# Performance work log

Hardware: AMD Instinct MI355X
Metric: run time of the kernel (lower is better)

The kernel has to match this reference:

```python
import jax, jax.numpy as jnp
import numpy as np

USAGE_DECAY = 0.99
EPS = 1e-12


def _addressing(key, beta, gate, shift, gamma, prev_w, memory, half_shift):
    # key [B,M], beta/gate/gamma [B,1], shift [B,K], prev_w [B,N], memory [B,N,M]
    kn = key / (jnp.linalg.norm(key, axis=-1, keepdims=True) + EPS)
    mn = memory / (jnp.linalg.norm(memory, axis=-1, keepdims=True) + EPS)
    cos = jnp.einsum('bnm,bm->bn', mn, kn)                      # [B,N]
    beta_p = jax.nn.softplus(beta[:, 0])
    wc = jax.nn.softmax(beta_p[:, None] * cos, axis=-1)
    g = jax.nn.sigmoid(gate[:, 0])[:, None]
    wg = g * wc + (1.0 - g) * prev_w
    s = jax.nn.softmax(shift, axis=-1)                          # [B,K]
    K = shift.shape[-1]
    shifted = sum(s[:, k:k + 1] * jnp.roll(wg, k - half_shift, axis=-1) for k in range(K))
    gamma_p = 1.0 + jax.nn.softplus(gamma[:, 0])
    wt = (shifted + EPS) ** gamma_p[:, None]
    return wt / (wt.sum(axis=-1, keepdims=True) + EPS)


def _allocate(usage):
    # faithful to source: cumprod over zero-prepended shifted usage
    sorted_u = jnp.sort(usage, axis=-1)
    free = jnp.argsort(usage, axis=-1)
    shifted = jnp.concatenate([jnp.zeros_like(sorted_u[:, :1]), sorted_u[:, :-1]], axis=-1)
    aw = (1.0 - sorted_u) * jnp.cumprod(shifted, axis=-1)
    B = usage.shape[0]
    return jnp.zeros_like(usage).at[jnp.arange(B)[:, None], free].set(aw)


def _forward(ctrl, read_W, read_b, write_W, write_b,
             memory0, link0, precedence0, usage0, read_w0, write_w0):
    T, B, D = ctrl.shape
    N, M = memory0.shape[1], memory0.shape[2]
    RH, WH = read_w0.shape[1], write_w0.shape[1]
    rpl = read_W.shape[0] // RH   # M + K + 6
    wpl = write_W.shape[0] // WH  # 3M + K + 4
    K = rpl - M - 6
    half = K // 2
    eye = jnp.eye(N, dtype=memory0.dtype)

    def step(carry, ctrl_t):
        memory, link, prec, usage, read_w, write_w = carry
        rp = (ctrl_t @ read_W.T + read_b).reshape(B, RH, rpl)
        wp = (ctrl_t @ write_W.T + write_b).reshape(B, WH, wpl)

        # ---- write heads: content addr + allocation, erase/add, temporal links ----
        new_write = []
        for h in range(WH):
            p = wp[:, h]
            key = p[:, :M]
            beta = p[:, M:M + 1]
            gate = p[:, M + 1:M + 2]
            shift = p[:, M + 2:M + 2 + K]
            gamma = p[:, M + 2 + K:M + 3 + K]
            erase = jax.nn.sigmoid(p[:, M + 3 + K:2 * M + 3 + K])
            add = p[:, 2 * M + 3 + K:3 * M + 3 + K]
            a_gate = jax.nn.sigmoid(p[:, 3 * M + 3 + K:])          # [B,1]
            w_addr = _addressing(key, beta, gate, shift, gamma, write_w[:, h], memory, half)
            alloc = _allocate(usage)
            w = a_gate * alloc + (1.0 - a_gate) * w_addr           # [B,N]
            memory = memory * (1.0 - w[:, :, None] * erase[:, None, :]) + w[:, :, None] * add[:, None, :]
            link = (1.0 - w[:, :, None]) * link + prec[:, :, None] * w[:, None, :]
            link = link * (1.0 - eye)[None]
            # faithful to source: sum over dim 0 (batch)
            prec = (1.0 - w.sum(axis=0, keepdims=True)) * prec + w
            usage = jnp.clip(USAGE_DECAY * usage + w, 0.0, 1.0)
            new_write.append(w)
        write_w = jnp.stack(new_write, axis=1)

        # ---- read heads: content + forward/backward temporal link modes ----
        new_read, reads = [], []
        for h in range(RH):
            p = rp[:, h]
            key = p[:, :M]
            beta = p[:, M:M + 1]
            gate = p[:, M + 1:M + 2]
            shift = p[:, M + 2:M + 2 + K]
            gamma = p[:, M + 2 + K:M + 3 + K]
            pi = jax.nn.softmax(p[:, M + 3 + K:M + 6 + K], axis=-1)  # [B,3] back/content/fwd
            wc = _addressing(key, beta, gate, shift, gamma, read_w[:, h], memory, half)
            fwd = jnp.einsum('bn,bnk->bk', read_w[:, h], link)
            bwd = jnp.einsum('bn,bkn->bk', read_w[:, h], link)
            w = pi[:, 0:1] * bwd + pi[:, 1:2] * wc + pi[:, 2:3] * fwd
            new_read.append(w)
            reads.append(jnp.einsum('bn,bnm->bm', w, memory))
        read_w = jnp.stack(new_read, axis=1)
        reads = jnp.stack(reads, axis=1)                            # [B,RH,M]
        return (memory, link, prec, usage, read_w, write_w), reads

    carry0 = (memory0, link0, precedence0, usage0, read_w0, write_w0)
    _, reads = jax.lax.scan(step, carry0, ctrl)
    return reads  # [T,B,RH,M]


def setup_inputs() -> dict:
    key = jax.random.key(0)
    ks = jax.random.split(key, 8)
    T, B, D = 32, 4, 256
    N, M = 1024, 256
    RH, WH, K = 1, 1, 3
    rpl = M + K + 6
    wpl = 3 * M + K + 4
    ctrl = jax.random.normal(ks[0], (T, B, D), dtype=jnp.float32)
    read_W = jax.random.normal(ks[1], (RH * rpl, D), dtype=jnp.float32) * 0.05
    read_b = jnp.zeros((RH * rpl,), dtype=jnp.float32)
    write_W = jax.random.normal(ks[2], (WH * wpl, D), dtype=jnp.float32) * 0.05
    write_b = jnp.zeros((WH * wpl,), dtype=jnp.float32)
    memory0 = jax.random.normal(ks[3], (B, N, M), dtype=jnp.float32) * 0.1
    link0 = jnp.zeros((B, N, N), dtype=jnp.float32)
    precedence0 = jnp.zeros((B, N), dtype=jnp.float32)
    usage0 = jax.random.uniform(ks[4], (B, N), dtype=jnp.float32)
    read_w0 = jnp.zeros((B, RH, N), dtype=jnp.float32).at[:, :, 0].set(1.0)
    write_w0 = jnp.zeros((B, WH, N), dtype=jnp.float32).at[:, :, 0].set(1.0)
    return {"ctrl": ctrl, "read_W": read_W, "read_b": read_b,
            "write_W": write_W, "write_b": write_b, "memory0": memory0,
            "link0": link0, "precedence0": precedence0, "usage0": usage0,
            "read_w0": read_w0, "write_w0": write_w0}


def reference(ctrl, read_W, read_b, write_W, write_b, memory0, link0,
              precedence0, usage0, read_w0, write_w0):
    return _forward(ctrl, read_W, read_b, write_W, write_b,
                    memory0, link0, precedence0, usage0, read_w0, write_w0)
```

## Files before the change

kernel.cpp:

```cpp
#include <hip/hip_runtime.h>

#define GRID 128
#define TPB 256
#define SLICE 32
#define BB 4
#define DD 256
#define NN 1024
#define MM 256
#define KSH 3
#define RPL 265
#define WPL 775
#define TS 32
#define EPSF 1e-12f

struct KArgs {
    const float *ctrl, *rW, *rb, *wW, *wb;
    const float *memory0, *prec0, *read_w0, *write_w0;
    float *out;
    float *rp, *wp;
    float *cosr, *cosw, *wbuf, *rdw;
    float *csp, *dsp;
    float *rdp;
    unsigned *flagsA, *flagsB;
};

__device__ __forceinline__ float cload(const float* p){
    return __hip_atomic_load(p, __ATOMIC_RELAXED, __HIP_MEMORY_SCOPE_SYSTEM);
}
__device__ __forceinline__ void cstore(float* p, float v){
    __hip_atomic_store(p, v, __ATOMIC_RELAXED, __HIP_MEMORY_SCOPE_SYSTEM);
}

__device__ __forceinline__ float softplusf(float x){
    return fmaxf(x, 0.0f) + log1pf(expf(-fabsf(x)));
}
__device__ __forceinline__ float sigmoidf(float x){
    return 1.0f / (1.0f + expf(-x));
}

template <bool FENCE>
__device__ __forceinline__ void garrive(unsigned* flags, unsigned gen, int g, int tid){
    __syncthreads();
    if (tid == 0){
        if (FENCE) __builtin_amdgcn_fence(__ATOMIC_RELEASE, "agent");
        __hip_atomic_store(&flags[g*16], gen, __ATOMIC_RELAXED, __HIP_MEMORY_SCOPE_SYSTEM);
    }
}
template <bool FENCE>
__device__ __forceinline__ void gwait(unsigned* flags, unsigned gen, int tid){
    if (tid < 64){
        while (1){
            unsigned f0 = __hip_atomic_load(&flags[tid*16], __ATOMIC_RELAXED, __HIP_MEMORY_SCOPE_SYSTEM);
            unsigned f1 = __hip_atomic_load(&flags[(tid+64)*16], __ATOMIC_RELAXED, __HIP_MEMORY_SCOPE_SYSTEM);
            if (__all(f0 >= gen && f1 >= gen)) break;
            __builtin_amdgcn_s_sleep(1);
        }
    }
    __syncthreads();
    if (FENCE) __builtin_amdgcn_fence(__ATOMIC_ACQUIRE, "agent");
    asm volatile("" ::: "memory");
}
__device__ __forceinline__ void gwaitA(unsigned* flags, unsigned gen, int b, int tid){
    if (tid < 64){
        int idx = b*32 + (tid & 31);
        while (1){
            unsigned f0 = __hip_atomic_load(&flags[idx*16], __ATOMIC_RELAXED, __HIP_MEMORY_SCOPE_SYSTEM);
            if (__all(f0 >= gen)) break;
            __builtin_amdgcn_s_sleep(1);
        }
    }
    __syncthreads();
    asm volatile("" ::: "memory");
}

__device__ __forceinline__ float blk_sum(float v, float* s4, int tid){
    #pragma unroll
    for (int off = 32; off; off >>= 1) v += __shfl_down(v, off);
    if ((tid & 63) == 0) s4[tid >> 6] = v;
    __syncthreads();
    float r = s4[0] + s4[1] + s4[2] + s4[3];
    __syncthreads();
    return r;
}

__device__ __forceinline__ float half_sum(float v, float* slots, int htid){
    #pragma unroll
    for (int off = 32; off; off >>= 1) v += __shfl_down(v, off);
    if ((htid & 63) == 0) slots[htid >> 6] = v;
    __syncthreads();
    float r = slots[0] + slots[1];
    __syncthreads();
    return r;
}

__device__ __forceinline__ void addr_core2(const float cosx[4], const float prev[4],
                                           const float* __restrict__ p,
                                           float* s4, float* wg, int tid,
                                           float out_wc[4]){
    float beta_p  = softplusf(p[MM]);
    float g       = sigmoidf(p[MM+1]);
    float s0r = p[MM+2], s1r = p[MM+3], s2r = p[MM+4];
    float smx = fmaxf(s0r, fmaxf(s1r, s2r));
    float e0 = expf(s0r-smx), e1 = expf(s1r-smx), e2 = expf(s2r-smx);
    float sden = e0+e1+e2;
    float s0 = e0/sden, s1 = e1/sden, s2 = e2/sden;
    float gamma_p = 1.0f + softplusf(p[MM+2+KSH]);
    float ev[4]; float ls = 0.0f;
    #pragma unroll
    for (int q = 0; q < 4; q++){ ev[q] = expf(beta_p*cosx[q] - beta_p); ls += ev[q]; }
    float bs = blk_sum(ls, s4, tid);
    float invb = 1.0f / bs;
    #pragma unroll
    for (int q = 0; q < 4; q++){
        int i = tid + q*256;
        wg[i] = g*(ev[q]*invb) + (1.0f-g)*prev[q];
    }
    __syncthreads();
    float wt[4]; float lps = 0.0f;
    #pragma unroll
    for (int q = 0; q < 4; q++){
        int i = tid + q*256;
        float sh = s0*wg[(i+1)&(NN-1)] + s1*wg[i] + s2*wg[(i-1)&(NN-1)];
        wt[q] = exp2f(gamma_p * log2f(sh + EPSF));
        lps += wt[q];
    }
    float ts = blk_sum(lps, s4, tid);
    float inv = 1.0f / (ts + EPSF);
    #pragma unroll
    for (int q = 0; q < 4; q++) out_wc[q] = wt[q] * inv;
    __syncthreads();
}

__device__ __forceinline__ void addr_half(const float cosx[8], const float prev[8],
                                          const float* __restrict__ p,
                                          float* swg, float* slots,
                                          int htid, float out_wc[8]){
    float beta_p  = softplusf(p[MM]);
    float g       = sigmoidf(p[MM+1]);
    float s0r = p[MM+2], s1r = p[MM+3], s2r = p[MM+4];
    float smx = fmaxf(s0r, fmaxf(s1r, s2r));
    float e0 = expf(s0r-smx), e1 = expf(s1r-smx), e2 = expf(s2r-smx);
    float sden = e0+e1+e2;
    float s0 = e0/sden, s1 = e1/sden, s2 = e2/sden;
    float gamma_p = 1.0f + softplusf(p[MM+2+KSH]);

    float ev[8]; float ls = 0.0f;
    #pragma unroll
    for (int q = 0; q < 8; q++){ ev[q] = expf(beta_p*cosx[q] - beta_p); ls += ev[q]; }
    float bs = half_sum(ls, slots, htid);
    float invb = 1.0f / bs;
    #pragma unroll
    for (int q = 0; q < 8; q++){
        int i = htid + q*128;
        swg[i] = g*(ev[q]*invb) + (1.0f-g)*prev[q];
    }
    __syncthreads();
    float wt[8]; float lps = 0.0f;
    #pragma unroll
    for (int q = 0; q < 8; q++){
        int i = htid + q*128;
        float sh = s0*swg[(i+1)&(NN-1)] + s1*swg[i] + s2*swg[(i-1)&(NN-1)];
        wt[q] = exp2f(gamma_p * log2f(sh + EPSF));
        lps += wt[q];
    }
    float ts2 = half_sum(lps, slots, htid);
    float inv = 1.0f / (ts2 + EPSF);
    #pragma unroll
    for (int q = 0; q < 8; q++) out_wc[q] = wt[q] * inv;
    __syncthreads();
}

__device__ __forceinline__ void tail_cos(const KArgs& a, int tnext, int b, int g, int ns0,
        float (*lmem)[MM], float (*skey)[MM],
        const float* lwn, const float* rdvec, int tid){
    if (rdvec){
        float accv = 0.f;
        #pragma unroll 8
        for (int j = 0; j < SLICE; j++) accv += rdvec[j]*lmem[j][tid];
        cstore(&a.rdp[(size_t)((tnext-1)&1)*GRID*MM + g*MM + tid], accv);
    }
    const float* kr = a.rp + (size_t)tnext*BB*RPL + (size_t)b*RPL;
    const bool hw = (tnext+1 <= TS-1);
    const float* kwp = a.wp + (size_t)(hw ? tnext+1 : tnext)*BB*WPL + (size_t)b*WPL;
    skey[0][tid] = kr[tid];
    skey[1][tid] = kwp[tid];
    __syncthreads();
    {
        const float* pw = a.wp + (size_t)tnext*BB*WPL + (size_t)b*WPL;
        float e = pw[MM+3+KSH + tid];
        float d = pw[2*MM+3+KSH + tid];
        #pragma unroll 8
        for (int j = 0; j < SLICE; j++){
            float w = lwn[j];
            lmem[j][tid] = lmem[j][tid]*(1.0f - w*e) + w*d;
        }
    }
    __syncthreads();
    {
        int j = tid >> 3, c = tid & 7;
        float dr=0.f, dw=0.f, nm=0.f, nr=0.f, nk=0.f;
        #pragma unroll
        for (int m = 0; m < 8; m++){
            int col = c*4 + m*32;
            float4 mv = *(const float4*)&lmem[j][col];
            float4 rv = *(const float4*)&skey[0][col];
            float4 wv = *(const float4*)&skey[1][col];
            dr += mv.x*rv.x + mv.y*rv.y + mv.z*rv.z + mv.w*rv.w;
            dw += mv.x*wv.x + mv.y*wv.y + mv.z*wv.z + mv.w*wv.w;
            nm += mv.x*mv.x + mv.y*mv.y + mv.z*mv.z + mv.w*mv.w;
            nr += rv.x*rv.x + rv.y*rv.y + rv.z*rv.z + rv.w*rv.w;
            nk += wv.x*wv.x + wv.y*wv.y + wv.z*wv.z + wv.w*wv.w;
        }
        #pragma unroll
        for (int off = 4; off; off >>= 1){
            dr += __shfl_down(dr, off); dw += __shfl_down(dw, off);
            nm += __shfl_down(nm, off); nr += __shfl_down(nr, off);
            nk += __shfl_down(nk, off);
        }
        if (c == 0){
            float sn = sqrtf(nm) + EPSF;
            int n = ns0 + j;
            cstore(&a.cosr[(size_t)(tnext&1)*BB*NN + b*NN + n], dr/(sn*(sqrtf(nr)+EPSF)));
            if (hw) cstore(&a.cosw[(size_t)((tnext+1)&1)*BB*NN + b*NN + n], dw/(sn*(sqrtf(nk)+EPSF)));
        }
    }
}

__device__ __forceinline__ void tail_links(const KArgs& a, int tnext, int g,
        float (*lA)[SLICE], float (*lW)[SLICE],
        const float* lwn, const float* rvec, const float* lprec, int tid){
    for (int p2 = tid; p2 < tnext*SLICE; p2 += TPB){
        int s = p2 >> 5, jj = p2 & 31;
        lA[s][jj] *= (1.0f - lwn[jj]);
    }
    __syncthreads();
    if (tid < SLICE){ lA[tnext][tid] = lprec[tid]; lW[tnext][tid] = lwn[tid]; }
    __syncthreads();
    int s = tid >> 3, c = tid & 7;
    if (s <= tnext){
        float pc = 0.f, pd = 0.f;
        #pragma unroll
        for (int q = 0; q < 4; q++){
            int jj = c*4 + q;
            float r = rvec[jj];
            pc += r*lA[s][jj];
            pd += r*lW[s][jj];
        }
        #pragma unroll
        for (int off = 4; off; off >>= 1){ pc += __shfl_down(pc, off); pd += __shfl_down(pd, off); }
        if (c == 0){
            cstore(&a.csp[(size_t)(tnext&1)*GRID*TS + g*TS + s], pc);
            cstore(&a.dsp[(size_t)(tnext&1)*GRID*TS + g*TS + s], pd);
        }
    }
}

__global__ void __launch_bounds__(TPB) kfull(KArgs a){
    const int g   = blockIdx.x;
    const int tid = threadIdx.x;
    const int wvi = tid >> 6, lane = tid & 63;
    const int b   = g >> 5;
    const int sl  = g & 31;
    const int ns0 = sl * SLICE;
    const int sq    = sl >> 3;
    const int sbase = (sl & 7) * 32;
    const int hbase = ns0 & 127;
    const int qsl   = ns0 >> 7;

    __shared__ __align__(16) float lmem[SLICE][MM];
    __shared__ __align__(16) float skey[2][MM];
    __shared__ __align__(16) float lA[TS][SLICE];
    __shared__ __align__(16) float lW[TS][SLICE];
    __shared__ float wgA[NN], wgB[NN];
    __shared__ float s8[8];
    __shared__ float scs[TS], sds[TS];
    __shared__ float lprec[SLICE], lr_old[SLICE], lw_old[SLICE];
    __shared__ float lrn[SLICE], lwn[SLICE], lbw[SLICE], lfw[SLICE];

    {
        const int tt = g >> 2;
        for (int o = tid; o < BB*DD; o += TPB) wgA[o] = a.ctrl[(size_t)tt*BB*DD + o];
        __syncthreads();
        for (int half = 0; half < 2; half++){
            int jc = (g & 3) + half*4;
            int j = jc*130 + tid;
            if (tid < 130 && j < RPL + WPL){
                const float* wrow; float bias; int isw, jj;
                if (j < RPL){ jj = j;       wrow = a.rW + (size_t)jj*DD; bias = a.rb[jj]; isw = 0; }
                else        { jj = j - RPL; wrow = a.wW + (size_t)jj*DD; bias = a.wb[jj]; isw = 1; }
                const float4* w4 = (const float4*)wrow;
                float a0 = bias, a1 = bias, a2 = bias, a3 = bias;
                for (int d = 0; d < DD/4; d++){
                    float4 wv = w4[d];
                    float4 c0 = *(const float4*)&wgA[0*DD + d*4];
                    float4 c1 = *(const float4*)&wgA[1*DD + d*4];
                    float4 c2 = *(const float4*)&wgA[2*DD + d*4];
                    float4 c3 = *(const float4*)&wgA[3*DD + d*4];
                    a0 += wv.x*c0.x + wv.y*c0.y + wv.z*c0.z + wv.w*c0.w;
                    a1 += wv.x*c1.x + wv.y*c1.y + wv.z*c1.z + wv.w*c1.w;
                    a2 += wv.x*c2.x + wv.y*c2.y + wv.z*c2.z + wv.w*c2.w;
                    a3 += wv.x*c3.x + wv.y*c3.y + wv.z*c3.z + wv.w*c3.w;
                }
                if (isw && jj >= MM+3+KSH && jj < 2*MM+3+KSH){
                    a0 = sigmoidf(a0); a1 = sigmoidf(a1); a2 = sigmoidf(a2); a3 = sigmoidf(a3);
                }
                if (!isw){
                    float* dst = a.rp + (size_t)tt*BB*RPL;
                    dst[0*RPL+jj]=a0; dst[1*RPL+jj]=a1; dst[2*RPL+jj]=a2; dst[3*RPL+jj]=a3;
                } else {
                    float* dst = a.wp + (size_t)tt*BB*WPL;
                    dst[0*WPL+jj]=a0; dst[1*WPL+jj]=a1; dst[2*WPL+jj]=a2; dst[3*WPL+jj]=a3;
                }
            }
        }
    }
    garrive<true>(a.flagsA, 1, g, tid);
    gwait<true>(a.flagsA, 1, tid);

    {
        const float* kw = a.wp + (size_t)b*WPL;
        const int m0 = lane*4;
        float k0=kw[m0], k1=kw[m0+1], k2=kw[m0+2], k3=kw[m0+3];
        float nk = k0*k0 + k1*k1 + k2*k2 + k3*k3;
        #pragma unroll
        for (int off = 32; off; off >>= 1) nk += __shfl_down(nk, off);
        nk = __shfl(nk, 0);
        float snk = sqrtf(nk) + EPSF;
        for (int rr = 0; rr < 8; rr++){
            int j = wvi*8 + rr, n = ns0 + j;
            float4 m4 = ((const float4*)a.memory0)[((size_t)(b*NN+n))*64 + lane];
            *(float4*)&lmem[j][m0] = m4;
            float dw = m4.x*k0 + m4.y*k1 + m4.z*k2 + m4.w*k3;
            float nm = m4.x*m4.x + m4.y*m4.y + m4.z*m4.z + m4.w*m4.w;
            #pragma unroll
            for (int off = 32; off; off >>= 1){ dw += __shfl_down(dw, off); nm += __shfl_down(nm, off); }
            if (lane == 0) cstore(&a.cosw[0*BB*NN + b*NN + n], dw / ((sqrtf(nm)+EPSF)*snk));
        }
        if (tid < SLICE){
            lprec[tid]  = a.prec0[b*NN + ns0 + tid];
            lr_old[tid] = a.read_w0[b*NN + ns0 + tid];
        }
    }
    garrive<false>(a.flagsA, 2, g, tid);
    gwait<false>(a.flagsA, 2, tid);

    {
        const float* p = a.wp + (size_t)b*WPL;
        float cosx[4], prev[4], wcf[4];
        #pragma unroll
        for (int q = 0; q < 4; q++){
            int i = tid + q*256;
            cosx[q] = cload(&a.cosw[0*BB*NN + b*NN + i]);
            prev[q] = a.write_w0[b*NN + i];
        }
        addr_core2(cosx, prev, p, s8, wgA, tid, wcf);
        float ag = sigmoidf(p[3*MM+3+KSH]);
        if (tid >= sbase && tid < sbase+32){
            int j = tid - sbase;
            float v = (1.0f - ag)*wcf[sq];
            lwn[j] = v;
            cstore(&a.wbuf[0*BB*NN + b*NN + ns0 + j], v);
        }
        __syncthreads();
        tail_cos(a, 0, b, g, ns0, lmem, skey, lwn, nullptr, tid);
        garrive<false>(a.flagsA, 3, g, tid);
        tail_links(a, 0, g, lA, lW, lwn, lr_old, lprec, tid);
        garrive<false>(a.flagsB, 1, g, tid);
        __syncthreads();
        if (tid < SLICE) lw_old[tid] = lwn[tid];
    }

    for (int t = 0; t < TS; t++){
        const int cur = t & 1, nxt = cur ^ 1;
        const int half = wvi >> 1, htid = tid & 127;
        gwaitA(a.flagsA, 3 + t, b, tid);

        float cosx[8], prev[8];
        const float* addr_p;
        if (half == 0){
            addr_p = a.rp + (size_t)t*BB*RPL + (size_t)b*RPL;
            #pragma unroll
            for (int q = 0; q < 8; q++){
                int i = htid + q*128;
                cosx[q] = cload(&a.cosr[(size_t)cur*BB*NN + b*NN + i]);
                prev[q] = (t == 0) ? a.read_w0[b*NN + i]
                                   : cload(&a.rdw[(size_t)nxt*BB*NN + b*NN + i]);
            }
        } else {
            int tw = (t < TS-1) ? t+1 : t;
            addr_p = a.wp + (size_t)tw*BB*WPL + (size_t)b*WPL;
            #pragma unroll
            for (int q = 0; q < 8; q++){
                int i = htid + q*128;
                cosx[q] = cload(&a.cosw[(size_t)nxt*BB*NN + b*NN + i]);
                prev[q] = cload(&a.wbuf[(size_t)cur*BB*NN + b*NN + i]);
            }
        }

        gwait<false>(a.flagsB, 1 + t, tid);

        float cv[4] = {0,0,0,0}, dv[4] = {0,0,0,0};
        {
            int s = tid >> 3, c = tid & 7;
            if (s <= t){
                #pragma unroll
                for (int q = 0; q < 4; q++){
                    int slc = c + q*8;
                    cv[q] = cload(&a.csp[(size_t)cur*GRID*TS + (b*32+slc)*TS + s]);
                    dv[q] = cload(&a.dsp[(size_t)cur*GRID*TS + (b*32+slc)*TS + s]);
                }
            }
        }
        float rdpv = 0.f;
        if (t > 0)
            rdpv = cload(&a.rdp[(size_t)nxt*GRID*MM + (size_t)(b*32+(tid&31))*MM + sl*8 + (tid>>5)]);
        if (tid < SLICE){
            float wsum = 0.f;
            #pragma unroll
            for (int bq = 0; bq < BB; bq++)
                wsum += cload(&a.wbuf[(size_t)cur*BB*NN + bq*NN + ns0 + tid]);
            lprec[tid] = (1.0f - wsum)*lprec[tid] + lw_old[tid];
        }

        float wcf[8];
        addr_half(cosx, prev, addr_p,
                  (half == 0) ? wgA : wgB,
                  (half == 0) ? &s8[0] : &s8[2],
                  htid, wcf);

        {
            int s = tid >> 3, c = tid & 7;
            float pc = cv[0]+cv[1]+cv[2]+cv[3];
            float pd = dv[0]+dv[1]+dv[2]+dv[3];
            #pragma unroll
            for (int off = 4; off; off >>= 1){ pc += __shfl_down(pc, off); pd += __shfl_down(pd, off); }
            if (c == 0 && s <= t){ scs[s] = pc; sds[s] = pd; }
            if (t > 0){
                #pragma unroll
                for (int off = 16; off; off >>= 1) rdpv += __shfl_down(rdpv, off);
                if ((tid & 31) == 0) a.out[(size_t)(t-1)*BB*MM + b*MM + sl*8 + (tid>>5)] = rdpv;
            }
        }
        __syncthreads();
        if (tid < SLICE){
            float bwv = 0.f, fwv = 0.f, qq = 0.f;
            for (int s2 = 0; s2 <= t; s2++){
                float av = lA[s2][tid], wv = lW[s2][tid];
                qq  += av*wv;
                bwv += sds[s2]*av;
                fwv += scs[s2]*wv;
            }
            float corr = lr_old[tid]*qq;
            lbw[tid] = bwv - corr;
            lfw[tid] = fwv - corr;
        }
        __syncthreads();
        if (half == 0){
            float x0 = addr_p[MM+3+KSH], x1 = addr_p[MM+4+KSH], x2 = addr_p[MM+5+KSH];
            float mx = fmaxf(x0, fmaxf(x1, x2));
            float q0 = expf(x0-mx), q1 = expf(x1-mx), q2 = expf(x2-mx);
            float qs = q0+q1+q2;
            float pi0 = q0/qs, pi1 = q1/qs, pi2 = q2/qs;
            if (htid >= hbase && htid < hbase + 32){
                int j = htid - hbase;
                float v = pi0*lbw[j] + pi1*wcf[qsl] + pi2*lfw[j];
                lrn[j] = v;
                cstore(&a.rdw[(size_t)cur*BB*NN + b*NN + ns0 + j], v);
            }
        } else if (t < TS-1){
            float ag = sigmoidf(addr_p[3*MM+3+KSH]);
            if (htid >= hbase && htid < hbase + 32){
                int j = htid - hbase;
                float v = (1.0f - ag)*wcf[qsl];
                lwn[j] = v;
                cstore(&a.wbuf[(size_t)nxt*BB*NN + b*NN + ns0 + j], v);
            }
        }
        __syncthreads();

        if (t < TS-1){
            tail_cos(a, t+1, b, g, ns0, lmem, skey, lwn, lrn, tid);
            garrive<false>(a.flagsA, 4 + t, g, tid);
            tail_links(a, t+1, g, lA, lW, lwn, lrn, lprec, tid);
            garrive<false>(a.flagsB, 2 + t, g, tid);
            __syncthreads();
            if (tid < SLICE){ lr_old[tid] = lrn[tid]; lw_old[tid] = lwn[tid]; }
        } else {
            float accv = 0.f;
            #pragma unroll 8
            for (int j = 0; j < SLICE; j++) accv += lrn[j]*lmem[j][tid];
            cstore(&a.rdp[(size_t)1*GRID*MM + g*MM + tid], accv);
            garrive<false>(a.flagsB, 2 + t, g, tid);
        }
    }

    gwait<false>(a.flagsB, TS + 1, tid);
    {
        float v = cload(&a.rdp[(size_t)1*GRID*MM + (size_t)(b*32+(tid&31))*MM + sl*8 + (tid>>5)]);
        #pragma unroll
        for (int off = 16; off; off >>= 1) v += __shfl_down(v, off);
        if ((tid & 31) == 0) a.out[(size_t)(TS-1)*BB*MM + b*MM + sl*8 + (tid>>5)] = v;
    }
}

extern "C" void kernel_launch(void* const* d_in, const int* in_sizes, int n_in,
                              void* d_out, int out_size, void* d_ws, size_t ws_size,
                              hipStream_t stream) {
    KArgs ka;
    ka.ctrl     = (const float*)d_in[0];
    ka.rW       = (const float*)d_in[1];
    ka.rb       = (const float*)d_in[2];
    ka.wW       = (const float*)d_in[3];
    ka.wb       = (const float*)d_in[4];
    ka.memory0  = (const float*)d_in[5];
    ka.prec0    = (const float*)d_in[7];
    ka.read_w0  = (const float*)d_in[9];
    ka.write_w0 = (const float*)d_in[10];
    ka.out      = (float*)d_out;

    float* ws = (float*)d_ws;
    size_t off = 0;
    auto alloc = [&](size_t n){ float* p = ws + off; off += n; return p; };
    ka.rp    = alloc((size_t)TS*BB*RPL);
    ka.wp    = alloc((size_t)TS*BB*WPL);
    ka.cosr  = alloc(2*(size_t)BB*NN);
    ka.cosw  = alloc(2*(size_t)BB*NN);
    ka.wbuf  = alloc(2*(size_t)BB*NN);
    ka.rdw   = alloc(2*(size_t)BB*NN);
    ka.csp   = alloc(2*(size_t)GRID*TS);
    ka.dsp   = alloc(2*(size_t)GRID*TS);
    ka.rdp   = alloc(2*(size_t)GRID*MM);
    unsigned* ubase = (unsigned*)(ws + off);
    ka.flagsA = ubase;
    ka.flagsB = ubase + GRID*16;
    size_t bar_bytes = (2*GRID*16) * sizeof(unsigned);

    hipMemsetAsync((void*)ubase, 0, bar_bytes, stream);
    void* params[] = { &ka };
    hipLaunchCooperativeKernel((const void*)kfull, dim3(GRID), dim3(TPB), params, 0, stream);
}
```

Baseline: 332.9 us.

## Specialize waves per task and replace block reductions with wave-level shuffles

The per-timestep phase is split across the four waves of each block. Wave 0 does read-head addressing, wave 1 does write-head addressing, wave 2 does link/precedence sums and wave 3 does readout and precedence. Each wave waits only on the grid flags it needs. Addressing over 1024 slots is now done within one wave (16 elements per lane) with xor-shuffle reductions and neighbour shuffles for the circular shift, which removes several __syncthreads and the shared wg buffers from the critical path. The cost is more serial work per lane and fewer active waves during addressing.

New measurement: 334.3 us. Within noise of the previous version (+0.4%).

```diff
diff --git a/kernel.cpp b/kernel.cpp
--- a/kernel.cpp
+++ b/kernel.cpp
@@ -60,16 +60,22 @@
     if (FENCE) __builtin_amdgcn_fence(__ATOMIC_ACQUIRE, "agent");
     asm volatile("" ::: "memory");
 }
-__device__ __forceinline__ void gwaitA(unsigned* flags, unsigned gen, int b, int tid){
-    if (tid < 64){
-        int idx = b*32 + (tid & 31);
-        while (1){
-            unsigned f0 = __hip_atomic_load(&flags[idx*16], __ATOMIC_RELAXED, __HIP_MEMORY_SCOPE_SYSTEM);
-            if (__all(f0 >= gen)) break;
-            __builtin_amdgcn_s_sleep(1);
-        }
-    }
-    __syncthreads();
+__device__ __forceinline__ void waitA_wave(unsigned* flags, unsigned gen, int b, int lane){
+    int idx = b*32 + (lane & 31);
+    while (1){
+        unsigned f = __hip_atomic_load(&flags[idx*16], __ATOMIC_RELAXED, __HIP_MEMORY_SCOPE_SYSTEM);
+        if (__all(f >= gen)) break;
+        __builtin_amdgcn_s_sleep(1);
+    }
+    asm volatile("" ::: "memory");
+}
+__device__ __forceinline__ void waitB_wave(unsigned* flags, unsigned gen, int lane){
+    while (1){
+        unsigned f0 = __hip_atomic_load(&flags[lane*16], __ATOMIC_RELAXED, __HIP_MEMORY_SCOPE_SYSTEM);
+        unsigned f1 = __hip_atomic_load(&flags[(lane+64)*16], __ATOMIC_RELAXED, __HIP_MEMORY_SCOPE_SYSTEM);
+        if (__all(f0 >= gen && f1 >= gen)) break;
+        __builtin_amdgcn_s_sleep(1);
+    }
     asm volatile("" ::: "memory");
 }
 
@@ -79,16 +85,6 @@
     if ((tid & 63) == 0) s4[tid >> 6] = v;
     __syncthreads();
     float r = s4[0] + s4[1] + s4[2] + s4[3];
-    __syncthreads();
-    return r;
-}
-
-__device__ __forceinline__ float half_sum(float v, float* slots, int htid){
-    #pragma unroll
-    for (int off = 32; off; off >>= 1) v += __shfl_down(v, off);
-    if ((htid & 63) == 0) slots[htid >> 6] = v;
-    __syncthreads();
-    float r = slots[0] + slots[1];
     __syncthreads();
     return r;
 }
@@ -131,10 +127,10 @@
     __syncthreads();
 }
 
-__device__ __forceinline__ void addr_half(const float cosx[8], const float prev[8],
-                                          const float* __restrict__ p,
-                                          float* swg, float* slots,
-                                          int htid, float out_wc[8]){
+__device__ __forceinline__ void wave_addr(const float* __restrict__ p,
+                                          const float* cos_src,
+                                          const float* prev_src, const float* prev_src0,
+                                          int use0, int lane, float out_w[16]){
     float beta_p  = softplusf(p[MM]);
     float g       = sigmoidf(p[MM+1]);
     float s0r = p[MM+2], s1r = p[MM+3], s2r = p[MM+4];
@@ -143,31 +139,37 @@
     float sden = e0+e1+e2;
     float s0 = e0/sden, s1 = e1/sden, s2 = e2/sden;
     float gamma_p = 1.0f + softplusf(p[MM+2+KSH]);
-
-    float ev[8]; float ls = 0.0f;
-    #pragma unroll
-    for (int q = 0; q < 8; q++){ ev[q] = expf(beta_p*cosx[q] - beta_p); ls += ev[q]; }
-    float bs = half_sum(ls, slots, htid);
-    float invb = 1.0f / bs;
-    #pragma unroll
-    for (int q = 0; q < 8; q++){
-        int i = htid + q*128;
-        swg[i] = g*(ev[q]*invb) + (1.0f-g)*prev[q];
-    }
-    __syncthreads();
-    float wt[8]; float lps = 0.0f;
-    #pragma unroll
-    for (int q = 0; q < 8; q++){
-        int i = htid + q*128;
-        float sh = s0*swg[(i+1)&(NN-1)] + s1*swg[i] + s2*swg[(i-1)&(NN-1)];
-        wt[q] = exp2f(gamma_p * log2f(sh + EPSF));
-        lps += wt[q];
-    }
-    float ts2 = half_sum(lps, slots, htid);
-    float inv = 1.0f / (ts2 + EPSF);
-    #pragma unroll
-    for (int q = 0; q < 8; q++) out_wc[q] = wt[q] * inv;
-    __syncthreads();
+    const int i0 = lane*16;
+    float ev[16], prev[16]; float ls = 0.0f;
+    #pragma unroll
+    for (int k = 0; k < 16; k++){
+        float cx = cload(&cos_src[i0+k]);
+        prev[k] = use0 ? prev_src0[i0+k] : cload(&prev_src[i0+k]);
+        ev[k] = expf(beta_p*cx - beta_p);
+        ls += ev[k];
+    }
+    #pragma unroll
+    for (int off = 32; off; off >>= 1) ls += __shfl_xor(ls, off);
+    float invb = 1.0f / ls;
+    float wg[16];
+    #pragma unroll
+    for (int k = 0; k < 16; k++) wg[k] = g*(ev[k]*invb) + (1.0f-g)*prev[k];
+    float wgL = __shfl(wg[15], (lane+63)&63);
+    float wgR = __shfl(wg[0],  (lane+ 1)&63);
+    float lps = 0.0f;
+    #pragma unroll
+    for (int k = 0; k < 16; k++){
+        float lv = (k == 0 ) ? wgL : wg[k-1];
+        float rv = (k == 15) ? wgR : wg[k+1];
+        float sh = s0*rv + s1*wg[k] + s2*lv;
+        out_w[k] = exp2f(gamma_p * log2f(sh + EPSF));
+        lps += out_w[k];
+    }
+    #pragma unroll
+    for (int off = 32; off; off >>= 1) lps += __shfl_xor(lps, off);
+    float inv = 1.0f / (lps + EPSF);
+    #pragma unroll
+    for (int k = 0; k < 16; k++) out_w[k] *= inv;
 }
 
 __device__ __forceinline__ void tail_cos(const KArgs& a, int tnext, int b, int g, int ns0,
@@ -264,16 +266,16 @@
     const int ns0 = sl * SLICE;
     const int sq    = sl >> 3;
     const int sbase = (sl & 7) * 32;
-    const int hbase = ns0 & 127;
-    const int qsl   = ns0 >> 7;
+    const int lbase = sl * 2;
 
     __shared__ __align__(16) float lmem[SLICE][MM];
     __shared__ __align__(16) float skey[2][MM];
     __shared__ __align__(16) float lA[TS][SLICE];
     __shared__ __align__(16) float lW[TS][SLICE];
-    __shared__ float wgA[NN], wgB[NN];
+    __shared__ float wgA[NN];
     __shared__ float s8[8];
-    __shared__ float scs[TS], sds[TS];
+    __shared__ float spi[4];
+    __shared__ float swcf_r[SLICE], swcf_w[SLICE];
     __shared__ float lprec[SLICE], lr_old[SLICE], lw_old[SLICE];
     __shared__ float lrn[SLICE], lwn[SLICE], lbw[SLICE], lfw[SLICE];
 
@@ -372,109 +374,102 @@
 
     for (int t = 0; t < TS; t++){
         const int cur = t & 1, nxt = cur ^ 1;
-        const int half = wvi >> 1, htid = tid & 127;
-        gwaitA(a.flagsA, 3 + t, b, tid);
-
-        float cosx[8], prev[8];
-        const float* addr_p;
-        if (half == 0){
-            addr_p = a.rp + (size_t)t*BB*RPL + (size_t)b*RPL;
-            #pragma unroll
-            for (int q = 0; q < 8; q++){
-                int i = htid + q*128;
-                cosx[q] = cload(&a.cosr[(size_t)cur*BB*NN + b*NN + i]);
-                prev[q] = (t == 0) ? a.read_w0[b*NN + i]
-                                   : cload(&a.rdw[(size_t)nxt*BB*NN + b*NN + i]);
-            }
-        } else {
-            int tw = (t < TS-1) ? t+1 : t;
-            addr_p = a.wp + (size_t)tw*BB*WPL + (size_t)b*WPL;
-            #pragma unroll
-            for (int q = 0; q < 8; q++){
-                int i = htid + q*128;
-                cosx[q] = cload(&a.cosw[(size_t)nxt*BB*NN + b*NN + i]);
-                prev[q] = cload(&a.wbuf[(size_t)cur*BB*NN + b*NN + i]);
-            }
-        }
-
-        gwait<false>(a.flagsB, 1 + t, tid);
-
-        float cv[4] = {0,0,0,0}, dv[4] = {0,0,0,0};
-        {
-            int s = tid >> 3, c = tid & 7;
+
+        if (wvi == 0){
+            waitA_wave(a.flagsA, 3 + t, b, lane);
+            const float* p = a.rp + (size_t)t*BB*RPL + (size_t)b*RPL;
+            float wloc[16];
+            wave_addr(p, a.cosr + (size_t)cur*BB*NN + b*NN,
+                      a.rdw + (size_t)nxt*BB*NN + b*NN,
+                      a.read_w0 + b*NN, (t == 0), lane, wloc);
+            if (lane == 0){
+                float x0 = p[MM+3+KSH], x1 = p[MM+4+KSH], x2 = p[MM+5+KSH];
+                float mx = fmaxf(x0, fmaxf(x1, x2));
+                float q0 = expf(x0-mx), q1 = expf(x1-mx), q2 = expf(x2-mx);
+                float qs = q0+q1+q2;
+                spi[0] = q0/qs; spi[1] = q1/qs; spi[2] = q2/qs;
+            }
+            if (lane == lbase || lane == lbase+1){
+                int j0 = (lane - lbase)*16;
+                #pragma unroll
+                for (int k = 0; k < 16; k++) swcf_r[j0+k] = wloc[k];
+            }
+        } else if (wvi == 1){
+            waitA_wave(a.flagsA, 3 + t, b, lane);
+            if (t < TS-1){
+                const float* p = a.wp + (size_t)(t+1)*BB*WPL + (size_t)b*WPL;
+                float wloc[16];
+                wave_addr(p, a.cosw + (size_t)nxt*BB*NN + b*NN,
+                          a.wbuf + (size_t)cur*BB*NN + b*NN,
+                          a.wbuf, 0, lane, wloc);
+                if (lane == 0) spi[3] = sigmoidf(p[3*MM+3+KSH]);
+                if (lane == lbase || lane == lbase+1){
+                    int j0 = (lane - lbase)*16;
+                    #pragma unroll
+                    for (int k = 0; k < 16; k++) swcf_w[j0+k] = wloc[k];
+                }
+            }
+        } else if (wvi == 2){
+            waitB_wave(a.flagsB, 1 + t, lane);
+            int s = lane & 31, hf = lane >> 5;
+            float pc = 0.f, pd = 0.f;
             if (s <= t){
                 #pragma unroll
-                for (int q = 0; q < 4; q++){
-                    int slc = c + q*8;
-                    cv[q] = cload(&a.csp[(size_t)cur*GRID*TS + (b*32+slc)*TS + s]);
-                    dv[q] = cload(&a.dsp[(size_t)cur*GRID*TS + (b*32+slc)*TS + s]);
+                for (int q2 = 0; q2 < 16; q2++){
+                    int slc = hf*16 + q2;
+                    pc += cload(&a.csp[(size_t)cur*GRID*TS + (size_t)(b*32+slc)*TS + s]);
+                    pd += cload(&a.dsp[(size_t)cur*GRID*TS + (size_t)(b*32+slc)*TS + s]);
                 }
             }
-        }
-        float rdpv = 0.f;
-        if (t > 0)
-            rdpv = cload(&a.rdp[(size_t)nxt*GRID*MM + (size_t)(b*32+(tid&31))*MM + sl*8 + (tid>>5)]);
-        if (tid < SLICE){
-            float wsum = 0.f;
-            #pragma unroll
-            for (int bq = 0; bq < BB; bq++)
-                wsum += cload(&a.wbuf[(size_t)cur*BB*NN + bq*NN + ns0 + tid]);
-            lprec[tid] = (1.0f - wsum)*lprec[tid] + lw_old[tid];
-        }
-
-        float wcf[8];
-        addr_half(cosx, prev, addr_p,
-                  (half == 0) ? wgA : wgB,
-                  (half == 0) ? &s8[0] : &s8[2],
-                  htid, wcf);
-
-        {
-            int s = tid >> 3, c = tid & 7;
-            float pc = cv[0]+cv[1]+cv[2]+cv[3];
-            float pd = dv[0]+dv[1]+dv[2]+dv[3];
-            #pragma unroll
-            for (int off = 4; off; off >>= 1){ pc += __shfl_down(pc, off); pd += __shfl_down(pd, off); }
-            if (c == 0 && s <= t){ scs[s] = pc; sds[s] = pd; }
-            if (t > 0){
-                #pragma unroll
-                for (int off = 16; off; off >>= 1) rdpv += __shfl_down(rdpv, off);
-                if ((tid & 31) == 0) a.out[(size_t)(t-1)*BB*MM + b*MM + sl*8 + (tid>>5)] = rdpv;
-            }
-        }
-        __syncthreads();
-        if (tid < SLICE){
+            pc += __shfl_xor(pc, 32);
+            pd += __shfl_xor(pd, 32);
+            int j = lane & 31;
             float bwv = 0.f, fwv = 0.f, qq = 0.f;
             for (int s2 = 0; s2 <= t; s2++){
-                float av = lA[s2][tid], wv = lW[s2][tid];
+                float av = lA[s2][j], wv = lW[s2][j];
                 qq  += av*wv;
-                bwv += sds[s2]*av;
-                fwv += scs[s2]*wv;
-            }
-            float corr = lr_old[tid]*qq;
-            lbw[tid] = bwv - corr;
-            lfw[tid] = fwv - corr;
+                bwv += __shfl(pd, s2)*av;
+                fwv += __shfl(pc, s2)*wv;
+            }
+            if (lane < 32){
+                float corr = lr_old[j]*qq;
+                lbw[j] = bwv - corr;
+                lfw[j] = fwv - corr;
+            }
+        } else {
+            waitB_wave(a.flagsB, 1 + t, lane);
+            if (t > 0){
+                float rv = 0.f;
+                #pragma unroll
+                for (int q2 = 0; q2 < 4; q2++){
+                    int slc = (lane>>3)*4 + q2;
+                    rv += cload(&a.rdp[(size_t)nxt*GRID*MM + (size_t)(b*32+slc)*MM + sl*8 + (lane&7)]);
+                }
+                rv += __shfl_down(rv, 32);
+                rv += __shfl_down(rv, 16);
+                rv += __shfl_down(rv, 8);
+                if (lane < 8) a.out[(size_t)(t-1)*BB*MM + b*MM + sl*8 + lane] = rv;
+            }
+            if (lane < 32){
+                float wsum = 0.f;
+                #pragma unroll
+                for (int bq = 0; bq < BB; bq++)
+                    wsum += cload(&a.wbuf[(size_t)cur*BB*NN + bq*NN + ns0 + lane]);
+                lprec[lane] = (1.0f - wsum)*lprec[lane] + lw_old[lane];
+            }
         }
         __syncthreads();
-        if (half == 0){
-            float x0 = addr_p[MM+3+KSH], x1 = addr_p[MM+4+KSH], x2 = addr_p[MM+5+KSH];
-            float mx = fmaxf(x0, fmaxf(x1, x2));
-            float q0 = expf(x0-mx), q1 = expf(x1-mx), q2 = expf(x2-mx);
-            float qs = q0+q1+q2;
-            float pi0 = q0/qs, pi1 = q1/qs, pi2 = q2/qs;
-            if (htid >= hbase && htid < hbase + 32){
-                int j = htid - hbase;
-                float v = pi0*lbw[j] + pi1*wcf[qsl] + pi2*lfw[j];
-                lrn[j] = v;
-                cstore(&a.rdw[(size_t)cur*BB*NN + b*NN + ns0 + j], v);
-            }
-        } else if (t < TS-1){
-            float ag = sigmoidf(addr_p[3*MM+3+KSH]);
-            if (htid >= hbase && htid < hbase + 32){
-                int j = htid - hbase;
-                float v = (1.0f - ag)*wcf[qsl];
-                lwn[j] = v;
-                cstore(&a.wbuf[(size_t)nxt*BB*NN + b*NN + ns0 + j], v);
-            }
+
+        if (tid < 32){
+            int j = tid;
+            float v = spi[0]*lbw[j] + spi[1]*swcf_r[j] + spi[2]*lfw[j];
+            lrn[j] = v;
+            cstore(&a.rdw[(size_t)cur*BB*NN + b*NN + ns0 + j], v);
+        } else if (tid >= 64 && tid < 96 && t < TS-1){
+            int j = tid - 64;
+            float v = (1.0f - spi[3])*swcf_w[j];
+            lwn[j] = v;
+            cstore(&a.wbuf[(size_t)nxt*BB*NN + b*NN + ns0 + j], v);
         }
         __syncthreads();
 
```
